# Optimization experiments

Hardware: AMD Instinct MI355X
Metric: run time of the kernel (lower is better)

## Reference

```python
import jax, jax.numpy as jnp
import numpy as np

IM_SIZE = (256, 256)
GRID_SIZE = (512, 512)
J = 6                    # numpoints per dim
L = 1024                 # table oversampling
ALPHA = 2.34 * J         # Kaiser-Bessel alpha (order 0)
CENTER = J * L // 2      # center index of the KB table
B, C, M = 2, 16, 409600  # batch, coils, k-space points


def _kb_ft(f, J_, alpha):
    """Fourier transform of the order-0 Kaiser-Bessel kernel (Fessler)."""
    z = np.sqrt((np.pi * J_ * f) ** 2 - alpha ** 2 + 0j)
    z = np.where(np.abs(z) < 1e-12, 1e-12, z)
    return np.real(J_ * np.sinh(z) / (z * np.i0(alpha)))


def _build_table(J_, L_, K, N, alpha):
    """Oversampled KB kernel table with the linear phase that centers the
    apodization at (N-1)/2 (torchkbnufft stores complex tables for this reason)."""
    u = (np.arange(J_ * L_ + 1) - J_ * L_ / 2.0) / L_  # grid-unit offsets in [-J/2, J/2]
    fr = np.sqrt(np.maximum(0.0, 1.0 - (2.0 * u / J_) ** 2))
    kb = np.where(np.abs(u) <= J_ / 2.0, np.i0(alpha * fr) / np.i0(alpha), 0.0)
    tab = kb * np.exp(-1j * (2.0 * np.pi / K) * u * (N - 1) / 2.0)
    return np.stack([tab.real, tab.imag]).astype(np.float32)


def setup_inputs():
    key = jax.random.key(0)
    k1, k2 = jax.random.split(key)
    x = jax.random.normal(k1, (B, C, 2) + IM_SIZE, dtype=jnp.float32)
    om = jax.random.uniform(k2, (B, 2, M), dtype=jnp.float32, minval=-jnp.pi, maxval=jnp.pi)
    scs = []
    for d in range(2):
        n = np.arange(IM_SIZE[d]) - (IM_SIZE[d] - 1) / 2.0
        scs.append(1.0 / _kb_ft(n / GRID_SIZE[d], J, ALPHA))
    sc = np.outer(scs[0], scs[1])
    scaling_coef = jnp.asarray(np.stack([sc, np.zeros_like(sc)]).astype(np.float32))
    table_0 = jnp.asarray(_build_table(J, L, GRID_SIZE[0], IM_SIZE[0], ALPHA))
    table_1 = jnp.asarray(_build_table(J, L, GRID_SIZE[1], IM_SIZE[1], ALPHA))
    n_shift = jnp.asarray(np.array([IM_SIZE[0] // 2, IM_SIZE[1] // 2], dtype=np.float32))
    return {"x": x, "om": om, "scaling_coef": scaling_coef,
            "table_0": table_0, "table_1": table_1, "n_shift": n_shift}


def reference(x, om, scaling_coef, table_0, table_1, n_shift):
    K0, K1 = GRID_SIZE
    # apodize by scaling coefficients, zero-pad to the oversampled grid, FFT
    xc = (x[:, :, 0] + 1j * x[:, :, 1]) * (scaling_coef[0] + 1j * scaling_coef[1])
    xc = jnp.pad(xc, ((0, 0), (0, 0), (0, K0 - IM_SIZE[0]), (0, K1 - IM_SIZE[1])))
    Gf = jnp.fft.fftn(xc, axes=(-2, -1)).reshape(xc.shape[0], xc.shape[1], K0 * K1)
    t0 = table_0[0] + 1j * table_0[1]
    t1 = table_1[0] + 1j * table_1[1]
    # fractional grid coordinates of the off-grid points
    tm0 = om[:, 0] * (K0 / (2.0 * jnp.pi))  # (B, M)
    tm1 = om[:, 1] * (K1 / (2.0 * jnp.pi))
    koff0 = jnp.floor(tm0 - J / 2.0).astype(jnp.int32) + 1
    koff1 = jnp.floor(tm1 - J / 2.0).astype(jnp.int32) + 1
    # per-dim table-lookup coefficients and wrapped grid indices
    c0, i0, c1, i1 = [], [], [], []
    for j in range(J):
        g0 = koff0 + j
        g1 = koff1 + j
        c0.append(t0[jnp.round((tm0 - g0) * L).astype(jnp.int32) + CENTER])
        c1.append(t1[jnp.round((tm1 - g1) * L).astype(jnp.int32) + CENTER])
        i0.append(jnp.mod(g0, K0))
        i1.append(jnp.mod(g1, K1))
    # separable J x J neighbor accumulation (matches Jlist loop in torchkbnufft)
    kdat = jnp.zeros((Gf.shape[0], Gf.shape[1], tm0.shape[-1]), dtype=Gf.dtype)
    for a in range(J):
        for b in range(J):
            idx = (i0[a] * K1 + i1[b])[:, None, :]          # (B, 1, M)
            vals = jnp.take_along_axis(Gf, idx, axis=2)     # (B, C, M) gather
            kdat = kdat + (c0[a] * c1[b])[:, None, :] * vals
    # fftshift phase
    phase = jnp.exp(1j * (om[:, 0] * n_shift[0] + om[:, 1] * n_shift[1]))
    kdat = kdat * phase[:, None, :]
    return jnp.stack([kdat.real, kdat.imag], axis=2)  # (B, C, 2, M)
```

## Files before the change

### kernel.cpp

```cpp
#include <hip/hip_runtime.h>
#include <math.h>

#define BB 2
#define CC 16
#define MM 409600
#define NI 256
#define JJ 6
#define TABLE_LEN 6145
#define CENTER 3072
#define TILE 16
#define TDIM 32
#define NTILES 1024
#define HALO 22
#define HSZ (HALO * HALO)
#define NBINS 2048
#define CAP 640
#define BINC_STRIDE 16
#define SC_PPB 4096
#define SC_THREADS 1024
#define SC_PPT 4
#define GRP 4
#define NGRP 4
#define SB_THREADS 256
#define SB_PPT 3

__global__ void fft512_row_fused(const float* __restrict__ x, const float* __restrict__ sc,
                                 float2* __restrict__ gf, int b) {
  __shared__ float2 bufA[512];
  __shared__ float2 bufB[512];
  int line = blockIdx.x;
  int c = line >> 9;
  int gi = line & 511;
  int t = threadIdx.x;
  float2* g = gf + (size_t)line * 512;
  if (gi >= NI) {
    g[t] = make_float2(0.f, 0.f);
    g[t + 256] = make_float2(0.f, 0.f);
    return;
  }
  const float* xb = x + (size_t)(b * CC + c) * 2 * NI * NI + gi * NI;
  float xr = xb[t];
  float xi = xb[NI * NI + t];
  const float* scb = sc + gi * NI;
  float sr = scb[t];
  float si = scb[NI * NI + t];
  bufA[t] = make_float2(xr * sr - xi * si, xr * si + xi * sr);
  bufA[t + 256] = make_float2(0.f, 0.f);
  __syncthreads();
  float2* X = bufA;
  float2* Y = bufB;
  const float C0 = -6.283185307179586f / 512.0f;
  #pragma unroll
  for (int k = 0; k < 9; ++k) {
    int s = 1 << k;
    float2 a = X[t];
    float2 bb = X[t + 256];
    int ps = t & ~(s - 1);
    float ang = C0 * (float)ps;
    float wr, wi;
    __sincosf(ang, &wi, &wr);
    int wbase = ((t >> k) << (k + 1)) | (t & (s - 1));
    float2 dif = make_float2(a.x - bb.x, a.y - bb.y);
    Y[wbase] = make_float2(a.x + bb.x, a.y + bb.y);
    Y[wbase + s] = make_float2(dif.x * wr - dif.y * wi, dif.x * wi + dif.y * wr);
    __syncthreads();
    float2* tmp = X; X = Y; Y = tmp;
  }
  g[t] = X[t];
  g[t + 256] = X[t + 256];
}

__global__ void fft512_col(float2* __restrict__ data) {
  __shared__ float2 bufA[512 * 8];
  __shared__ float2 bufB[512 * 8];
  int blk = blockIdx.x;
  int img = blk >> 6;
  int cg = blk & 63;
  float2* g = data + ((size_t)img << 18) + cg * 8;
  int t = threadIdx.x;
  int col = t & 7;
  int r0 = t >> 3;
  #pragma unroll
  for (int k = 0; k < 4; ++k) {
    int row = r0 + 128 * k;
    bufA[row * 8 + col] = g[(size_t)row * 512 + col];
  }
  __syncthreads();
  float2* X = bufA;
  float2* Y = bufB;
  const float C0 = -6.283185307179586f / 512.0f;
  #pragma unroll
  for (int k = 0; k < 9; ++k) {
    int s = 1 << k;
    #pragma unroll
    for (int h = 0; h < 2; ++h) {
      int j = r0 + 128 * h;
      float2 a = X[j * 8 + col];
      float2 b = X[(j + 256) * 8 + col];
      int ps = j & ~(s - 1);
      float ang = C0 * (float)ps;
      float wr, wi;
      __sincosf(ang, &wi, &wr);
      int wbase = ((j >> k) << (k + 1)) | (j & (s - 1));
      float2 dif = make_float2(a.x - b.x, a.y - b.y);
      Y[wbase * 8 + col] = make_float2(a.x + b.x, a.y + b.y);
      Y[(wbase + s) * 8 + col] = make_float2(dif.x * wr - dif.y * wi, dif.x * wi + dif.y * wr);
    }
    __syncthreads();
    float2* tmp = X; X = Y; Y = tmp;
  }
  #pragma unroll
  for (int k = 0; k < 4; ++k) {
    int row = r0 + 128 * k;
    g[(size_t)row * 512 + col] = X[row * 8 + col];
  }
}

__global__ void build_tab(const float* __restrict__ t0, const float* __restrict__ t1,
                          float2* __restrict__ tab0, float2* __restrict__ tab1) {
  int i = blockIdx.x * blockDim.x + threadIdx.x;
  if (i < TABLE_LEN) {
    tab0[i] = make_float2(t0[i], t0[TABLE_LEN + i]);
    tab1[i] = make_float2(t1[i], t1[TABLE_LEN + i]);
  }
}

__global__ void zero_bins(int* __restrict__ binc) {
  int t = blockIdx.x * blockDim.x + threadIdx.x;
  if (t < NBINS * BINC_STRIDE) binc[t] = 0;
}

__global__ void scatter_points(const float* __restrict__ om,
                               int* __restrict__ binc,
                               float2* __restrict__ bpts, int* __restrict__ invcap) {
  __shared__ int lhist[NBINS];
  __shared__ int lbase[NBINS];
  __shared__ int lpos[NBINS];
  int t = threadIdx.x;
  int bid = blockIdx.x;
  for (int i = t; i < NBINS; i += SC_THREADS) { lhist[i] = 0; lpos[i] = 0; }
  __syncthreads();
  const float scale = 81.48733086305042f;
  float ptm0[SC_PPT], ptm1[SC_PPT];
  int pbin[SC_PPT];
  #pragma unroll
  for (int i = 0; i < SC_PPT; ++i) {
    int idx = bid * SC_PPB + i * SC_THREADS + t;
    int b = idx / MM;
    int m = idx - b * MM;
    float om0 = om[(size_t)b * 2 * MM + m];
    float om1 = om[(size_t)b * 2 * MM + MM + m];
    float tm0 = om0 * scale;
    float tm1 = om1 * scale;
    int s0 = ((int)floorf(tm0 - 3.0f) + 1) & 511;
    int s1 = ((int)floorf(tm1 - 3.0f) + 1) & 511;
    int bin = b * NTILES + (s0 >> 4) * TDIM + (s1 >> 4);
    ptm0[i] = tm0; ptm1[i] = tm1;
    pbin[i] = bin;
    atomicAdd(&lhist[bin], 1);
  }
  __syncthreads();
  for (int i = t; i < NBINS; i += SC_THREADS)
    lbase[i] = atomicAdd(&binc[i * BINC_STRIDE], lhist[i]);
  __syncthreads();
  #pragma unroll
  for (int i = 0; i < SC_PPT; ++i) {
    int idx = bid * SC_PPB + i * SC_THREADS + t;
    int bin = pbin[i];
    int pos = atomicAdd(&lpos[bin], 1);
    int slot = lbase[bin] + pos;
    if (slot < CAP) {
      bpts[bin * CAP + slot] = make_float2(ptm0[i], ptm1[i]);
    }
    int sl = slot < CAP ? slot : CAP - 1;
    invcap[idx] = (bin << 10) | sl;
  }
}

__global__ void prefix_bins(const int* __restrict__ binc, int* __restrict__ dbase) {
  __shared__ int buf[NBINS];
  int t = threadIdx.x;
  int c0 = binc[t * BINC_STRIDE];
  c0 = c0 < 0 ? 0 : (c0 > CAP ? CAP : c0);
  int c1 = binc[(NTILES + t) * BINC_STRIDE];
  c1 = c1 < 0 ? 0 : (c1 > CAP ? CAP : c1);
  buf[t] = c0;
  buf[NTILES + t] = c1;
  __syncthreads();
  for (int off = 1; off < NTILES; off <<= 1) {
    int v0 = (t >= off) ? buf[t - off] : 0;
    int v1 = (t >= off) ? buf[NTILES + t - off] : 0;
    __syncthreads();
    buf[t] += v0;
    buf[NTILES + t] += v1;
    __syncthreads();
  }
  dbase[t] = buf[t] - c0;
  dbase[NTILES + t] = buf[NTILES + t] - c1;
}

__global__ void sort_bins(float2* __restrict__ bpts, const int* __restrict__ binc,
                          unsigned short* __restrict__ perm) {
  __shared__ int hist[256];
  int bin = blockIdx.x;
  int t = threadIdx.x;
  int n = binc[bin * BINC_STRIDE];
  n = n < 0 ? 0 : (n > CAP ? CAP : n);
  hist[t] = 0;
  __syncthreads();
  float2 pts[SB_PPT];
  int keys[SB_PPT];
  #pragma unroll
  for (int i = 0; i < SB_PPT; ++i) {
    int p = t + i * SB_THREADS;
    keys[i] = -1;
    if (p < n) {
      float2 pt = bpts[bin * CAP + p];
      int d0 = (((int)floorf(pt.x - 3.0f)) + 1) & 15;
      int d1 = (((int)floorf(pt.y - 3.0f)) + 1) & 15;
      keys[i] = (d0 << 4) | d1;
      pts[i] = pt;
      atomicAdd(&hist[keys[i]], 1);
    }
  }
  __syncthreads();
  int c = hist[t];
  for (int off = 1; off < 256; off <<= 1) {
    int u = (t >= off) ? hist[t - off] : 0;
    __syncthreads();
    hist[t] += u;
    __syncthreads();
  }
  int excl = hist[t] - c;
  __syncthreads();
  hist[t] = excl;
  __syncthreads();
  #pragma unroll
  for (int i = 0; i < SB_PPT; ++i) {
    if (keys[i] >= 0) {
      int np = atomicAdd(&hist[keys[i]], 1);
      bpts[bin * CAP + np] = pts[i];
      perm[bin * CAP + (t + i * SB_THREADS)] = (unsigned short)np;
    }
  }
}

__global__ void __launch_bounds__(256, 4)
interp_binned(const float2* __restrict__ gf,
              const float2* __restrict__ bpts,
              const int* __restrict__ binc,
              const int* __restrict__ dbase,
              const float2* __restrict__ tab0,
              const float2* __restrict__ tab1,
              float2* __restrict__ tmp, int b) {
  __shared__ float2 lds[GRP * HSZ];
  int blk = blockIdx.x;
  int grp = blk & (NGRP - 1);
  int tile = blk >> 2;
  int cbase = grp * GRP;
  int tile0 = tile >> 5, tile1 = tile & 31;
  int base0 = tile0 * TILE, base1 = tile1 * TILE;
  int tid = threadIdx.x;
  for (int i = tid; i < GRP * HSZ; i += 256) {
    int cc = i / HSZ;
    int rem = i - cc * HSZ;
    int r = rem / HALO;
    int cl = rem - r * HALO;
    const float2* img = gf + ((size_t)(cbase + cc) << 18);
    lds[i] = img[(((base0 + r) & 511) << 9) | ((base1 + cl) & 511)];
  }
  __syncthreads();
  int bin = b * NTILES + tile;
  int count = binc[bin * BINC_STRIDE];
  count = count < 0 ? 0 : (count > CAP ? CAP : count);
  int pbase = bin * CAP;
  int dbin = dbase[bin];
  for (int p = tid; p < count; p += 256) {
    float2 pt = bpts[pbase + p];
    float tm0 = pt.x, tm1 = pt.y;
    int koff0 = (int)floorf(tm0 - 3.0f) + 1;
    int koff1 = (int)floorf(tm1 - 3.0f) + 1;
    int d0 = koff0 & 15;
    int d1 = koff1 & 15;
    float c0r[JJ], c0i[JJ], c1r[JJ], c1i[JJ];
    #pragma unroll
    for (int j = 0; j < JJ; ++j) {
      int idx0 = (int)rintf((tm0 - (float)(koff0 + j)) * 1024.0f) + CENTER;
      idx0 = idx0 < 0 ? 0 : (idx0 > TABLE_LEN - 1 ? TABLE_LEN - 1 : idx0);
      float2 v0 = tab0[idx0];
      c0r[j] = v0.x; c0i[j] = v0.y;
      int idx1 = (int)rintf((tm1 - (float)(koff1 + j)) * 1024.0f) + CENTER;
      idx1 = idx1 < 0 ? 0 : (idx1 > TABLE_LEN - 1 ? TABLE_LEN - 1 : idx1);
      float2 v1 = tab1[idx1];
      c1r[j] = v1.x; c1i[j] = v1.y;
    }
    float2 res[GRP];
    #pragma unroll
    for (int g = 0; g < GRP; ++g) {
      const float2* hal = lds + g * HSZ;
      float ar = 0.f, ai = 0.f;
      #pragma unroll
      for (int ja = 0; ja < JJ; ++ja) {
        const float2* row = hal + (d0 + ja) * HALO + d1;
        float rr = 0.f, ri = 0.f;
        #pragma unroll
        for (int jb = 0; jb < JJ; ++jb) {
          float2 v = row[jb];
          rr += c1r[jb] * v.x - c1i[jb] * v.y;
          ri += c1r[jb] * v.y + c1i[jb] * v.x;
        }
        ar += c0r[ja] * rr - c0i[ja] * ri;
        ai += c0r[ja] * ri + c0i[ja] * rr;
      }
      res[g] = make_float2(ar, ai);
    }
    float4* d4 = (float4*)(tmp + ((size_t)grp * MM + (dbin + p)) * GRP);
    d4[0] = make_float4(res[0].x, res[0].y, res[1].x, res[1].y);
    d4[1] = make_float4(res[2].x, res[2].y, res[3].x, res[3].y);
  }
}

__global__ void gather_out(const float2* __restrict__ tmp, const int* __restrict__ invcap,
                           const int* __restrict__ dbase, const unsigned short* __restrict__ perm,
                           const float* __restrict__ om,
                           const float* __restrict__ nshift, float* __restrict__ out, int b) {
  int m = blockIdx.x * blockDim.x + threadIdx.x;
  if (m >= MM) return;
  int v = invcap[b * MM + m];
  int bin = v >> 10;
  int pos = v & 1023;
  int slot = dbase[bin] + (int)perm[bin * CAP + pos];
  float om0 = om[(size_t)b * 2 * MM + m];
  float om1 = om[(size_t)b * 2 * MM + MM + m];
  float ph = om0 * nshift[0] + om1 * nshift[1];
  float sp, cp;
  sincosf(ph, &sp, &cp);
  float* ob = out + (size_t)b * CC * 2 * MM + m;
  #pragma unroll
  for (int g = 0; g < NGRP; ++g) {
    const float4* src = (const float4*)(tmp + ((size_t)g * MM + slot) * GRP);
    float4 v0 = src[0];
    float4 v1 = src[1];
    int c = g * GRP;
    ob[(size_t)(2 * c + 0) * MM] = v0.x * cp - v0.y * sp;
    ob[(size_t)(2 * c + 1) * MM] = v0.x * sp + v0.y * cp;
    ob[(size_t)(2 * c + 2) * MM] = v0.z * cp - v0.w * sp;
    ob[(size_t)(2 * c + 3) * MM] = v0.z * sp + v0.w * cp;
    ob[(size_t)(2 * c + 4) * MM] = v1.x * cp - v1.y * sp;
    ob[(size_t)(2 * c + 5) * MM] = v1.x * sp + v1.y * cp;
    ob[(size_t)(2 * c + 6) * MM] = v1.z * cp - v1.w * sp;
    ob[(size_t)(2 * c + 7) * MM] = v1.z * sp + v1.w * cp;
  }
}

extern "C" void kernel_launch(void* const* d_in, const int* in_sizes, int n_in,
                              void* d_out, int out_size, void* d_ws, size_t ws_size,
                              hipStream_t stream) {
  const float* x = (const float*)d_in[0];
  const float* om = (const float*)d_in[1];
  const float* sc = (const float*)d_in[2];
  const float* t0 = (const float*)d_in[3];
  const float* t1 = (const float*)d_in[4];
  const float* nshift = (const float*)d_in[5];
  float* out = (float*)d_out;

  char* ws = (char*)d_ws;
  float2* gf = (float2*)ws;
  size_t off = (size_t)CC * 512 * 512 * sizeof(float2);
  float2* bpts = (float2*)(ws + off); off += (size_t)NBINS * CAP * sizeof(float2);
  float2* tmp = (float2*)(ws + off);  off += (size_t)MM * CC * sizeof(float2);
  int* invcap = (int*)(ws + off);     off += (size_t)BB * MM * sizeof(int);
  unsigned short* perm = (unsigned short*)(ws + off); off += (size_t)NBINS * CAP * sizeof(unsigned short);
  float2* tab0 = (float2*)(ws + off); off += (size_t)TABLE_LEN * sizeof(float2);
  float2* tab1 = (float2*)(ws + off); off += (size_t)TABLE_LEN * sizeof(float2);
  int* binc = (int*)(ws + off);       off += (size_t)NBINS * BINC_STRIDE * sizeof(int);
  int* dbase = (int*)(ws + off);      off += (size_t)NBINS * sizeof(int);

  build_tab<<<(TABLE_LEN + 255) / 256, 256, 0, stream>>>(t0, t1, tab0, tab1);
  zero_bins<<<(NBINS * BINC_STRIDE + 255) / 256, 256, 0, stream>>>(binc);
  scatter_points<<<BB * MM / SC_PPB, SC_THREADS, 0, stream>>>(om, binc, bpts, invcap);
  prefix_bins<<<1, NTILES, 0, stream>>>(binc, dbase);
  sort_bins<<<NBINS, SB_THREADS, 0, stream>>>(bpts, binc, perm);
  for (int b = 0; b < BB; ++b) {
    fft512_row_fused<<<CC * 512, 256, 0, stream>>>(x, sc, gf, b);
    fft512_col<<<CC * 64, 1024, 0, stream>>>(gf);
    interp_binned<<<NTILES * NGRP, 256, 0, stream>>>(gf, bpts, binc, dbase, tab0, tab1, tmp, b);
    gather_out<<<MM / 256, 256, 0, stream>>>(tmp, invcap, dbase, perm, om, nshift, out, b);
  }
}
```

Measured before the change: 478.5 us.

## Skip zero-padded FFT rows, widen interp coil group, merge prep kernels

```diff
diff --git a/kernel.cpp b/kernel.cpp
--- a/kernel.cpp
+++ b/kernel.cpp
@@ -19,8 +19,10 @@
 #define SC_PPB 4096
 #define SC_THREADS 1024
 #define SC_PPT 4
-#define GRP 4
-#define NGRP 4
+#define GRP 8
+#define NGRP 2
+#define PC 4
+#define NPL 4
 #define SB_THREADS 256
 #define SB_PPT 3
 
@@ -29,15 +31,10 @@
   __shared__ float2 bufA[512];
   __shared__ float2 bufB[512];
   int line = blockIdx.x;
-  int c = line >> 9;
-  int gi = line & 511;
-  int t = threadIdx.x;
-  float2* g = gf + (size_t)line * 512;
-  if (gi >= NI) {
-    g[t] = make_float2(0.f, 0.f);
-    g[t + 256] = make_float2(0.f, 0.f);
-    return;
-  }
+  int c = line >> 8;
+  int gi = line & 255;
+  int t = threadIdx.x;
+  float2* g = gf + (((size_t)c << 9) | gi) * 512;
   const float* xb = x + (size_t)(b * CC + c) * 2 * NI * NI + gi * NI;
   float xr = xb[t];
   float xi = xb[NI * NI + t];
@@ -81,9 +78,14 @@
   int col = t & 7;
   int r0 = t >> 3;
   #pragma unroll
-  for (int k = 0; k < 4; ++k) {
+  for (int k = 0; k < 2; ++k) {
     int row = r0 + 128 * k;
     bufA[row * 8 + col] = g[(size_t)row * 512 + col];
+  }
+  #pragma unroll
+  for (int k = 2; k < 4; ++k) {
+    int row = r0 + 128 * k;
+    bufA[row * 8 + col] = make_float2(0.f, 0.f);
   }
   __syncthreads();
   float2* X = bufA;
@@ -116,18 +118,15 @@
   }
 }
 
-__global__ void build_tab(const float* __restrict__ t0, const float* __restrict__ t1,
-                          float2* __restrict__ tab0, float2* __restrict__ tab1) {
+__global__ void prep(const float* __restrict__ t0, const float* __restrict__ t1,
+                     float2* __restrict__ tab0, float2* __restrict__ tab1,
+                     int* __restrict__ binc) {
   int i = blockIdx.x * blockDim.x + threadIdx.x;
   if (i < TABLE_LEN) {
     tab0[i] = make_float2(t0[i], t0[TABLE_LEN + i]);
     tab1[i] = make_float2(t1[i], t1[TABLE_LEN + i]);
   }
-}
-
-__global__ void zero_bins(int* __restrict__ binc) {
-  int t = blockIdx.x * blockDim.x + threadIdx.x;
-  if (t < NBINS * BINC_STRIDE) binc[t] = 0;
+  if (i < NBINS * BINC_STRIDE) binc[i] = 0;
 }
 
 __global__ void scatter_points(const float* __restrict__ om,
@@ -245,7 +244,7 @@
   }
 }
 
-__global__ void __launch_bounds__(256, 4)
+__global__ void __launch_bounds__(256, 3)
 interp_binned(const float2* __restrict__ gf,
               const float2* __restrict__ bpts,
               const int* __restrict__ binc,
@@ -256,7 +255,7 @@
   __shared__ float2 lds[GRP * HSZ];
   int blk = blockIdx.x;
   int grp = blk & (NGRP - 1);
-  int tile = blk >> 2;
+  int tile = blk >> 1;
   int cbase = grp * GRP;
   int tile0 = tile >> 5, tile1 = tile & 31;
   int base0 = tile0 * TILE, base1 = tile1 * TILE;
@@ -314,9 +313,12 @@
       }
       res[g] = make_float2(ar, ai);
     }
-    float4* d4 = (float4*)(tmp + ((size_t)grp * MM + (dbin + p)) * GRP);
-    d4[0] = make_float4(res[0].x, res[0].y, res[1].x, res[1].y);
-    d4[1] = make_float4(res[2].x, res[2].y, res[3].x, res[3].y);
+    float4* dA = (float4*)(tmp + ((size_t)(2 * grp) * MM + (dbin + p)) * PC);
+    dA[0] = make_float4(res[0].x, res[0].y, res[1].x, res[1].y);
+    dA[1] = make_float4(res[2].x, res[2].y, res[3].x, res[3].y);
+    float4* dB = (float4*)(tmp + ((size_t)(2 * grp + 1) * MM + (dbin + p)) * PC);
+    dB[0] = make_float4(res[4].x, res[4].y, res[5].x, res[5].y);
+    dB[1] = make_float4(res[6].x, res[6].y, res[7].x, res[7].y);
   }
 }
 
@@ -334,14 +336,14 @@
   float om1 = om[(size_t)b * 2 * MM + MM + m];
   float ph = om0 * nshift[0] + om1 * nshift[1];
   float sp, cp;
-  sincosf(ph, &sp, &cp);
+  __sincosf(ph, &sp, &cp);
   float* ob = out + (size_t)b * CC * 2 * MM + m;
   #pragma unroll
-  for (int g = 0; g < NGRP; ++g) {
-    const float4* src = (const float4*)(tmp + ((size_t)g * MM + slot) * GRP);
+  for (int g = 0; g < NPL; ++g) {
+    const float4* src = (const float4*)(tmp + ((size_t)g * MM + slot) * PC);
     float4 v0 = src[0];
     float4 v1 = src[1];
-    int c = g * GRP;
+    int c = g * PC;
     ob[(size_t)(2 * c + 0) * MM] = v0.x * cp - v0.y * sp;
     ob[(size_t)(2 * c + 1) * MM] = v0.x * sp + v0.y * cp;
     ob[(size_t)(2 * c + 2) * MM] = v0.z * cp - v0.w * sp;
@@ -376,13 +378,12 @@
   int* binc = (int*)(ws + off);       off += (size_t)NBINS * BINC_STRIDE * sizeof(int);
   int* dbase = (int*)(ws + off);      off += (size_t)NBINS * sizeof(int);
 
-  build_tab<<<(TABLE_LEN + 255) / 256, 256, 0, stream>>>(t0, t1, tab0, tab1);
-  zero_bins<<<(NBINS * BINC_STRIDE + 255) / 256, 256, 0, stream>>>(binc);
+  prep<<<(NBINS * BINC_STRIDE + 255) / 256, 256, 0, stream>>>(t0, t1, tab0, tab1, binc);
   scatter_points<<<BB * MM / SC_PPB, SC_THREADS, 0, stream>>>(om, binc, bpts, invcap);
   prefix_bins<<<1, NTILES, 0, stream>>>(binc, dbase);
   sort_bins<<<NBINS, SB_THREADS, 0, stream>>>(bpts, binc, perm);
   for (int b = 0; b < BB; ++b) {
-    fft512_row_fused<<<CC * 512, 256, 0, stream>>>(x, sc, gf, b);
+    fft512_row_fused<<<CC * 256, 256, 0, stream>>>(x, sc, gf, b);
     fft512_col<<<CC * 64, 1024, 0, stream>>>(gf);
     interp_binned<<<NTILES * NGRP, 256, 0, stream>>>(gf, bpts, binc, dbase, tab0, tab1, tmp, b);
     gather_out<<<MM / 256, 256, 0, stream>>>(tmp, invcap, dbase, perm, om, nshift, out, b);
```

New measurement: 558.0 us. 16.6% more time.
